# Kernel tuning notes

Hardware: AMD Instinct MI355X
Metric: run time of the kernel (lower is better)

## Reference

```python
import jax, jax.numpy as jnp
import numpy as np

EMBED = 1024
HEADS = 16
DK = EMBED // HEADS
DFF = 4 * EMBED
EPS = 1e-5


def layer_norm(x, g, b):
    mu = jnp.mean(x, axis=-1, keepdims=True)
    var = jnp.var(x, axis=-1, keepdims=True)
    return (x - mu) * jax.lax.rsqrt(var + EPS) * g + b


def setup_inputs() -> dict:
    key = jax.random.key(0)
    ks = jax.random.split(key, 12)
    s = lambda d: 1.0 / np.sqrt(d)
    return {
        "x": jax.random.normal(ks[0], (4, 1024, EMBED), dtype=jnp.float32),
        "norm_g": jnp.ones((EMBED,), jnp.float32),
        "norm_b": jnp.zeros((EMBED,), jnp.float32),
        "w_qkv": jax.random.normal(ks[1], (EMBED, 3 * EMBED), jnp.float32) * s(EMBED),
        "b_qkv": jnp.zeros((3 * EMBED,), jnp.float32),
        "w_proj": jax.random.normal(ks[2], (EMBED, EMBED), jnp.float32) * s(EMBED),
        "b_proj": jnp.zeros((EMBED,), jnp.float32),
        "w_fc1": jax.random.normal(ks[3], (EMBED, DFF), jnp.float32) * s(EMBED),
        "b_fc1": jnp.zeros((DFF,), jnp.float32),
        "w_fc2": jax.random.normal(ks[4], (DFF, EMBED), jnp.float32) * s(DFF),
        "b_fc2": jnp.zeros((EMBED,), jnp.float32),
    }


def reference(x, norm_g, norm_b, w_qkv, b_qkv, w_proj, b_proj, w_fc1, b_fc1, w_fc2, b_fc2):
    B, N, C = x.shape
    # --- attention branch (pre-norm, shared norm params) ---
    h = layer_norm(x, norm_g, norm_b)
    qkv = (h @ w_qkv + b_qkv).reshape(B, N, 3, HEADS, DK)
    q, k, v = jnp.moveaxis(qkv, 2, 0)  # each [B, N, H, dk]
    # NOTE: source divides by dk**(-0.5), i.e. multiplies scores by sqrt(dk)
    scores = jnp.einsum('bnhd,bmhd->bhnm', q, k) * (DK ** 0.5)
    attn = jax.nn.softmax(scores, axis=-1)
    ctx = jnp.einsum('bhnm,bmhd->bnhd', attn, v).reshape(B, N, C)
    x = x + (ctx @ w_proj + b_proj)
    # --- MLP branch ---
    h = layer_norm(x, norm_g, norm_b)
    h = jax.nn.gelu(h @ w_fc1 + b_fc1, approximate=False)
    x = x + (h @ w_fc2 + b_fc2)
    return x
```

## Files before the change

### kernel.cpp

```cpp
#include <hip/hip_runtime.h>
#include <hip/hip_bf16.h>

typedef __attribute__((ext_vector_type(8))) short short8;
typedef __attribute__((ext_vector_type(8))) _Float16 half8;
typedef __attribute__((ext_vector_type(4))) float f32x4;

__device__ __forceinline__ unsigned short f2h(float f) {
    _Float16 h = (_Float16)f;
    return *reinterpret_cast<unsigned short*>(&h);
}
__device__ __forceinline__ float h2f(unsigned short u) {
    _Float16 h = *reinterpret_cast<_Float16*>(&u);
    return (float)h;
}

__device__ __forceinline__ void gld_lds16(const unsigned short* g, unsigned short* l) {
    __builtin_amdgcn_global_load_lds(
        (const __attribute__((address_space(1))) unsigned int*)g,
        (__attribute__((address_space(3))) unsigned int*)l, 16, 0, 0);
}

__global__ __launch_bounds__(256)
void transpose_all(const float* __restrict__ W0, const float* __restrict__ W1,
                   const float* __restrict__ W2, const float* __restrict__ W3,
                   unsigned short* __restrict__ o0, unsigned short* __restrict__ o1,
                   unsigned short* __restrict__ o2, unsigned short* __restrict__ o3) {
    __shared__ float tile[32][33];
    const int bid = blockIdx.x;
    const float* W; unsigned short* out; int K, N, loc;
    if (bid < 3072)      { W = W0; out = o0; K = 1024; N = 3072; loc = bid; }
    else if (bid < 4096) { W = W1; out = o1; K = 1024; N = 1024; loc = bid - 3072; }
    else if (bid < 8192) { W = W2; out = o2; K = 1024; N = 4096; loc = bid - 4096; }
    else                 { W = W3; out = o3; K = 4096; N = 1024; loc = bid - 8192; }
    const int nx = N >> 5;
    const int n0 = (loc % nx) << 5, k0 = (loc / nx) << 5;
    const int tid = threadIdx.x;
    const int r = tid >> 3, c4 = (tid & 7) << 2;
    float4 v = *reinterpret_cast<const float4*>(W + (size_t)(k0 + r) * N + n0 + c4);
    tile[r][c4 + 0] = v.x; tile[r][c4 + 1] = v.y;
    tile[r][c4 + 2] = v.z; tile[r][c4 + 3] = v.w;
    __syncthreads();
    const int n = n0 + r;
    ushort4 o;
    o.x = f2h(tile[c4 + 0][r]); o.y = f2h(tile[c4 + 1][r]);
    o.z = f2h(tile[c4 + 2][r]); o.w = f2h(tile[c4 + 3][r]);
    *reinterpret_cast<ushort4*>(out + (size_t)n * K + k0 + c4) = o;
}

__global__ __launch_bounds__(256)
void ln_kernel(const float* __restrict__ x, const float* __restrict__ gw,
               const float* __restrict__ bw, unsigned short* __restrict__ out) {
    const int row = blockIdx.x, tid = threadIdx.x;
    const float* xr = x + (size_t)row * 1024;
    float4 v = *reinterpret_cast<const float4*>(xr + tid * 4);
    float s = v.x + v.y + v.z + v.w;
    float sq = v.x * v.x + v.y * v.y + v.z * v.z + v.w * v.w;
    #pragma unroll
    for (int off = 1; off < 64; off <<= 1) {
        s  += __shfl_xor(s, off);
        sq += __shfl_xor(sq, off);
    }
    __shared__ float ps[4], pq[4];
    const int wave = tid >> 6;
    if ((tid & 63) == 0) { ps[wave] = s; pq[wave] = sq; }
    __syncthreads();
    s  = ps[0] + ps[1] + ps[2] + ps[3];
    sq = pq[0] + pq[1] + pq[2] + pq[3];
    const float mu = s * (1.0f / 1024.0f);
    const float var = sq * (1.0f / 1024.0f) - mu * mu;
    const float rs = rsqrtf(var + 1e-5f);
    float4 gv = *reinterpret_cast<const float4*>(gw + tid * 4);
    float4 bv = *reinterpret_cast<const float4*>(bw + tid * 4);
    ushort4 o;
    o.x = f2h((v.x - mu) * rs * gv.x + bv.x);
    o.y = f2h((v.y - mu) * rs * gv.y + bv.y);
    o.z = f2h((v.z - mu) * rs * gv.z + bv.z);
    o.w = f2h((v.w - mu) * rs * gv.w + bv.w);
    *reinterpret_cast<ushort4*>(out + (size_t)row * 1024 + tid * 4) = o;
}

template<int EPI>
__global__ __launch_bounds__(512, 4)
void gemm_mid(const unsigned short* __restrict__ A, const unsigned short* __restrict__ Bt,
              const float* __restrict__ bias, void* Cout,
              int M, int N, int K, int lda, int ldb, int ldc) {
    __shared__ unsigned short As[2][128 * 32];
    __shared__ unsigned short Bs[2][256 * 32];
    const int tid = threadIdx.x;
    const int wave = tid >> 6, lane = tid & 63;
    const int nwg = gridDim.x;
    const int swz = (blockIdx.x & 7) * (nwg >> 3) + (blockIdx.x >> 3);
    const int nx = N >> 8;
    const int bm = (swz / nx) << 7, bn = (swz % nx) << 8;
    const int wm = wave >> 2, wn = wave & 3;
    const int fr = lane & 15, g8 = (lane >> 4) << 3, fq = (lane >> 4) << 2;
    const int jq = g8 >> 3;
    const int sx2 = (fr >> 1) & 3;

    const int srow = lane >> 2;
    const int scol = ((lane & 3) ^ ((lane >> 3) & 3)) << 3;
    const unsigned short* gA  = A + (size_t)(bm + wave * 16 + srow) * lda + scol;
    const unsigned short* gB0 = Bt + (size_t)(bn + wave * 32 + srow) * ldb + scol;
    const unsigned short* gB1 = gB0 + (size_t)16 * ldb;
    const int lbA = wave * 512;
    const int lbB = wave * 1024;

    f32x4 acc[4][4];
    #pragma unroll
    for (int m = 0; m < 4; ++m)
        #pragma unroll
        for (int n_ = 0; n_ < 4; ++n_)
            #pragma unroll
            for (int r_ = 0; r_ < 4; ++r_) acc[m][n_][r_] = 0.0f;

    auto stage = [&](int buf, int k0) {
        gld_lds16(gA + k0, &As[buf][lbA]);
        gld_lds16(gB0 + k0, &Bs[buf][lbB]);
        gld_lds16(gB1 + k0, &Bs[buf][lbB + 512]);
    };
    auto compute = [&](int buf) {
        half8 af[4], bfv[4];
        #pragma unroll
        for (int m = 0; m < 4; ++m)
            af[m] = *reinterpret_cast<const half8*>(
                &As[buf][(wm * 64 + m * 16 + fr) * 32 + ((jq ^ sx2) << 3)]);
        #pragma unroll
        for (int n_ = 0; n_ < 4; ++n_)
            bfv[n_] = *reinterpret_cast<const half8*>(
                &Bs[buf][(wn * 64 + n_ * 16 + fr) * 32 + ((jq ^ sx2) << 3)]);
        #pragma unroll
        for (int m = 0; m < 4; ++m)
            #pragma unroll
            for (int n_ = 0; n_ < 4; ++n_)
                acc[m][n_] = __builtin_amdgcn_mfma_f32_16x16x32_f16(af[m], bfv[n_], acc[m][n_], 0, 0, 0);
    };

    const int nt = K >> 5;
    stage(0, 0);
    __syncthreads();
    int k0 = 32;
    for (int t = 0; t < nt - 2; t += 2) {
        stage(1, k0);
        compute(0);
        __syncthreads();
        stage(0, k0 + 32);
        compute(1);
        __syncthreads();
        k0 += 64;
    }
    stage(1, k0);
    compute(0);
    __syncthreads();
    compute(1);

    unsigned short* o16 = reinterpret_cast<unsigned short*>(Cout);
    #pragma unroll
    for (int n_ = 0; n_ < 4; ++n_) {
        const int col = bn + wn * 64 + n_ * 16 + fr;
        const float bc = bias[col];
        #pragma unroll
        for (int m = 0; m < 4; ++m) {
            #pragma unroll
            for (int r_ = 0; r_ < 4; ++r_) {
                const int row = bm + wm * 64 + m * 16 + fq + r_;
                const size_t idx = (size_t)row * ldc + col;
                float v = acc[m][n_][r_] + bc;
                if (EPI == 0) {
                    o16[idx] = f2h(v);
                } else {
                    float ge = 0.5f * v * (1.0f + erff(v * 0.70710678118654752f));
                    o16[idx] = f2h(ge);
                }
            }
        }
    }
}

template<int EPI, int BM>
__global__ __launch_bounds__(256)
void gemm_bt(const unsigned short* __restrict__ A, const unsigned short* __restrict__ Bt,
             const float* __restrict__ bias, const float* resid,
             void* Cout, int M, int N, int K, int lda, int ldb, int ldc) {
    constexpr int MF = BM / 32;
    __shared__ unsigned short As[2][BM * 32];
    __shared__ unsigned short Bs[2][128 * 32];
    const int tid = threadIdx.x;
    const int wave = tid >> 6, lane = tid & 63;
    const int bm = blockIdx.y * BM, bn = blockIdx.x << 7;
    const int wr = (wave >> 1) * (BM / 2), wc = (wave & 1) << 6;
    const int fr = lane & 15, g8 = (lane >> 4) << 3, fq = (lane >> 4) << 2;
    const int jq = g8 >> 3, sx2 = (fr >> 1) & 3;
    const size_t koff = (EPI >= 3) ? (size_t)blockIdx.z * K : 0;

    const int srowA = (BM == 128) ? ((wave << 5) + (lane >> 2)) : ((wave << 4) + (lane >> 2));
    const int srowB = (wave << 5) + (lane >> 2);
    const int scol = (((lane & 3) ^ ((lane >> 3) & 3))) << 3;
    const unsigned short* gA0 = A + (size_t)(bm + srowA) * lda + scol + koff;
    const unsigned short* gA1 = gA0 + (size_t)16 * lda;
    const unsigned short* gB0 = Bt + (size_t)(bn + srowB) * ldb + scol + koff;
    const unsigned short* gB1 = gB0 + (size_t)16 * ldb;

    f32x4 acc[MF][4];
    #pragma unroll
    for (int m = 0; m < MF; ++m)
        #pragma unroll
        for (int n = 0; n < 4; ++n)
            #pragma unroll
            for (int r = 0; r < 4; ++r) acc[m][n][r] = 0.0f;

    auto stage = [&](int buf, int k0) {
        unsigned short* lA = &As[buf][(BM == 128) ? (wave << 10) : (wave << 9)];
        unsigned short* lB = &Bs[buf][wave << 10];
        gld_lds16(gA0 + k0, lA);
        if constexpr (BM == 128) gld_lds16(gA1 + k0, lA + 512);
        gld_lds16(gB0 + k0, lB);
        gld_lds16(gB1 + k0, lB + 512);
    };
    auto compute = [&](int buf) {
        half8 af[MF], bfv[4];
        #pragma unroll
        for (int m = 0; m < MF; ++m)
            af[m] = *reinterpret_cast<const half8*>(
                &As[buf][(wr + m * 16 + fr) * 32 + ((jq ^ sx2) << 3)]);
        #pragma unroll
        for (int n = 0; n < 4; ++n)
            bfv[n] = *reinterpret_cast<const half8*>(
                &Bs[buf][(wc + n * 16 + fr) * 32 + ((jq ^ sx2) << 3)]);
        #pragma unroll
        for (int m = 0; m < MF; ++m)
            #pragma unroll
            for (int n = 0; n < 4; ++n)
                acc[m][n] = __builtin_amdgcn_mfma_f32_16x16x32_f16(af[m], bfv[n], acc[m][n], 0, 0, 0);
    };

    const int nt = K >> 5;
    stage(0, 0);
    __syncthreads();
    int k0 = 32;
    for (int t = 0; t < nt - 2; t += 2) {
        stage(1, k0);
        compute(0);
        __syncthreads();
        stage(0, k0 + 32);
        compute(1);
        __syncthreads();
        k0 += 64;
    }
    stage(1, k0);
    compute(0);
    __syncthreads();
    compute(1);

    if (EPI == 4) {
        unsigned short* P = reinterpret_cast<unsigned short*>(Cout) +
                            (size_t)blockIdx.z * (size_t)M * ldc;
        #pragma unroll
        for (int n = 0; n < 4; ++n) {
            const int col = bn + wc + n * 16 + fr;
            #pragma unroll
            for (int m = 0; m < MF; ++m)
                #pragma unroll
                for (int r = 0; r < 4; ++r) {
                    const int row = bm + wr + m * 16 + fq + r;
                    P[(size_t)row * ldc + col] = f2h(acc[m][n][r]);
                }
        }
        return;
    }

    #pragma unroll
    for (int n = 0; n < 4; ++n) {
        const int col = bn + wc + n * 16 + fr;
        const float bc = bias[col];
        #pragma unroll
        for (int m = 0; m < MF; ++m) {
            #pragma unroll
            for (int r = 0; r < 4; ++r) {
                const int row = bm + wr + m * 16 + fq + r;
                const size_t idx = (size_t)row * ldc + col;
                float v = acc[m][n][r] + bc;
                reinterpret_cast<float*>(Cout)[idx] = v + resid[idx];
            }
        }
    }
}

template<int Z>
__global__ __launch_bounds__(256)
void red_h(const unsigned short* __restrict__ p, const float* __restrict__ bias,
           float* out) {
    const size_t MN = (size_t)4096 * 1024;
    const size_t i = ((size_t)blockIdx.x * 256 + threadIdx.x) * 4;
    float4 r  = *reinterpret_cast<const float4*>(out + i);
    float4 bb = *reinterpret_cast<const float4*>(bias + (i & 1023));
    float o0 = r.x + bb.x, o1 = r.y + bb.y, o2 = r.z + bb.z, o3 = r.w + bb.w;
    #pragma unroll
    for (int z = 0; z < Z; ++z) {
        ushort4 a = *reinterpret_cast<const ushort4*>(p + (size_t)z * MN + i);
        o0 += h2f(a.x); o1 += h2f(a.y); o2 += h2f(a.z); o3 += h2f(a.w);
    }
    float4 o; o.x = o0; o.y = o1; o.z = o2; o.w = o3;
    *reinterpret_cast<float4*>(out + i) = o;
}

__global__ __launch_bounds__(256)
void kv_conv(const unsigned short* __restrict__ qkv16, unsigned short* __restrict__ K_g,
             unsigned short* __restrict__ Vt_g) {
    __shared__ unsigned short VtT[64][72];
    const int kc = blockIdx.x;
    const int bh = blockIdx.y;
    const int b = bh >> 4, h = bh & 15;
    const int tid = threadIdx.x;
    const int key = tid >> 2, c16 = (tid & 3) << 4;
    const unsigned short* kp = qkv16 + ((size_t)(b * 1024 + kc * 64 + key)) * 3072 + 1024 + h * 64 + c16;
    alignas(16) unsigned short kbuf[16];
    #pragma unroll
    for (int j = 0; j < 16; j += 8) {
        short8 k8 = *reinterpret_cast<const short8*>(kp + j);
        short8 v8 = *reinterpret_cast<const short8*>(kp + 1024 + j);
        #pragma unroll
        for (int c = 0; c < 8; ++c) {
            kbuf[j + c] = f2h(8.0f * h2f((unsigned short)k8[c]));
            VtT[c16 + j + c][key] = (unsigned short)v8[c];
        }
    }
    const size_t kb = ((size_t)bh * 1024 + kc * 64 + key) * 64 + c16;
    *reinterpret_cast<short8*>(K_g + kb)     = *reinterpret_cast<short8*>(&kbuf[0]);
    *reinterpret_cast<short8*>(K_g + kb + 8) = *reinterpret_cast<short8*>(&kbuf[8]);
    __syncthreads();
    const int d = tid >> 2;
    const size_t vb = ((size_t)bh * 64 + d) * 1024 + (size_t)kc * 64 + c16;
    *reinterpret_cast<short8*>(Vt_g + vb)     = *reinterpret_cast<const short8*>(&VtT[d][c16]);
    *reinterpret_cast<short8*>(Vt_g + vb + 8) = *reinterpret_cast<const short8*>(&VtT[d][c16 + 8]);
}

__global__ __launch_bounds__(256)
void attn_kernel(const unsigned short* __restrict__ qkv16,
                 const unsigned short* __restrict__ K_g,
                 const unsigned short* __restrict__ Vt_g,
                 unsigned short* __restrict__ ctx) {
    __shared__ unsigned short Kh[64][72];
    __shared__ unsigned short Vt[64][72];
    __shared__ unsigned short Plds[4][16][72];
    const int qt = blockIdx.x;
    const int bh = blockIdx.y;
    const int b = bh >> 4, h = bh & 15;
    const int tid = threadIdx.x;
    const int wave = tid >> 6, lane = tid & 63;
    const int fr = lane & 15, g8 = (lane >> 4) << 3, fq = (lane >> 4) << 2;

    const int qrow = qt * 64 + wave * 16 + fr;
    const unsigned short* qp = qkv16 + ((size_t)(b * 1024 + qrow)) * 3072 + h * 64;
    half8 qf[2];
    qf[0] = *reinterpret_cast<const half8*>(qp + g8);
    qf[1] = *reinterpret_cast<const half8*>(qp + 32 + g8);

    float mrun[4], lrun[4];
    f32x4 cacc[4];
    #pragma unroll
    for (int r = 0; r < 4; ++r) { mrun[r] = -3.0e38f; lrun[r] = 0.0f; }
    #pragma unroll
    for (int nd = 0; nd < 4; ++nd)
        #pragma unroll
        for (int r = 0; r < 4; ++r) cacc[nd][r] = 0.0f;

    const int skey = tid >> 2, sc16 = (tid & 3) << 4;
    const unsigned short* kgp = K_g + ((size_t)bh * 1024 + skey) * 64 + sc16;
    const unsigned short* vgp = Vt_g + ((size_t)bh * 64 + skey) * 1024 + sc16;

    short8 ka = *reinterpret_cast<const short8*>(kgp);
    short8 kb = *reinterpret_cast<const short8*>(kgp + 8);
    short8 va = *reinterpret_cast<const short8*>(vgp);
    short8 vb = *reinterpret_cast<const short8*>(vgp + 8);

    for (int kt = 0; kt < 16; ++kt) {
        __syncthreads();
        *reinterpret_cast<short8*>(&Kh[skey][sc16])     = ka;
        *reinterpret_cast<short8*>(&Kh[skey][sc16 + 8]) = kb;
        *reinterpret_cast<short8*>(&Vt[skey][sc16])     = va;
        *reinterpret_cast<short8*>(&Vt[skey][sc16 + 8]) = vb;
        __syncthreads();
        const int ktn = (kt < 15) ? kt + 1 : 15;
        ka = *reinterpret_cast<const short8*>(kgp + (size_t)ktn * 4096);
        kb = *reinterpret_cast<const short8*>(kgp + (size_t)ktn * 4096 + 8);
        va = *reinterpret_cast<const short8*>(vgp + ktn * 64);
        vb = *reinterpret_cast<const short8*>(vgp + ktn * 64 + 8);

        f32x4 S[4];
        #pragma unroll
        for (int n = 0; n < 4; ++n)
            #pragma unroll
            for (int r = 0; r < 4; ++r) S[n][r] = 0.0f;
        #pragma unroll
        for (int s_ = 0; s_ < 2; ++s_)
            #pragma unroll
            for (int n = 0; n < 4; ++n) {
                half8 kh = *reinterpret_cast<const half8*>(&Kh[n * 16 + fr][s_ * 32 + g8]);
                S[n] = __builtin_amdgcn_mfma_f32_16x16x32_f16(qf[s_], kh, S[n], 0, 0, 0);
            }

        float mt[4];
        #pragma unroll
        for (int r = 0; r < 4; ++r)
            mt[r] = fmaxf(fmaxf(S[0][r], S[1][r]), fmaxf(S[2][r], S[3][r]));
        #pragma unroll
        for (int r = 0; r < 4; ++r) {
            mt[r] = fmaxf(mt[r], __shfl_xor(mt[r], 1));
            mt[r] = fmaxf(mt[r], __shfl_xor(mt[r], 2));
            mt[r] = fmaxf(mt[r], __shfl_xor(mt[r], 4));
            mt[r] = fmaxf(mt[r], __shfl_xor(mt[r], 8));
        }
        float P[4][4], rsum[4];
        #pragma unroll
        for (int r = 0; r < 4; ++r) {
            float mnew = fmaxf(mrun[r], mt[r]);
            float sf = __expf(mrun[r] - mnew);
            mrun[r] = mnew;
            rsum[r] = 0.0f;
            #pragma unroll
            for (int n = 0; n < 4; ++n) {
                float p = __expf(S[n][r] - mnew);
                P[n][r] = p;
                rsum[r] += p;
            }
            lrun[r] *= sf;
            #pragma unroll
            for (int nd = 0; nd < 4; ++nd) cacc[nd][r] *= sf;
        }
        #pragma unroll
        for (int r = 0; r < 4; ++r) {
            rsum[r] += __shfl_xor(rsum[r], 1);
            rsum[r] += __shfl_xor(rsum[r], 2);
            rsum[r] += __shfl_xor(rsum[r], 4);
            rsum[r] += __shfl_xor(rsum[r], 8);
            lrun[r] += rsum[r];
        }
        #pragma unroll
        for (int n = 0; n < 4; ++n)
            #pragma unroll
            for (int r = 0; r < 4; ++r)
                Plds[wave][fq + r][n * 16 + fr] = f2h(P[n][r]);
        #pragma unroll
        for (int s_ = 0; s_ < 2; ++s_) {
            half8 pa = *reinterpret_cast<const half8*>(&Plds[wave][fr][s_ * 32 + g8]);
            #pragma unroll
            for (int nd = 0; nd < 4; ++nd) {
                half8 vb8 = *reinterpret_cast<const half8*>(&Vt[nd * 16 + fr][s_ * 32 + g8]);
                cacc[nd] = __builtin_amdgcn_mfma_f32_16x16x32_f16(pa, vb8, cacc[nd], 0, 0, 0);
            }
        }
    }
    #pragma unroll
    for (int r = 0; r < 4; ++r) {
        const float inv = 1.0f / lrun[r];
        const int row = qt * 64 + wave * 16 + fq + r;
        unsigned short* cp = ctx + ((size_t)(b * 1024 + row)) * 1024 + h * 64;
        #pragma unroll
        for (int nd = 0; nd < 4; ++nd)
            cp[nd * 16 + fr] = f2h(cacc[nd][r] * inv);
    }
}

extern "C" void kernel_launch(void* const* d_in, const int* in_sizes, int n_in,
                              void* d_out, int out_size, void* d_ws, size_t ws_size,
                              hipStream_t stream) {
    const float* x      = (const float*)d_in[0];
    const float* norm_g = (const float*)d_in[1];
    const float* norm_b = (const float*)d_in[2];
    const float* w_qkv  = (const float*)d_in[3];
    const float* b_qkv  = (const float*)d_in[4];
    const float* w_proj = (const float*)d_in[5];
    const float* b_proj = (const float*)d_in[6];
    const float* w_fc1  = (const float*)d_in[7];
    const float* b_fc1  = (const float*)d_in[8];
    const float* w_fc2  = (const float*)d_in[9];
    const float* b_fc2  = (const float*)d_in[10];
    float* out = (float*)d_out;
    char* ws = (char*)d_ws;

    size_t off = 0;
    unsigned short* wqkvT  = (unsigned short*)(ws + off); off += (size_t)3072 * 1024 * 2;
    unsigned short* wprojT = (unsigned short*)(ws + off); off += (size_t)1024 * 1024 * 2;
    unsigned short* wfc1T  = (unsigned short*)(ws + off); off += (size_t)4096 * 1024 * 2;
    unsigned short* wfc2T  = (unsigned short*)(ws + off); off += (size_t)1024 * 4096 * 2;
    unsigned short* ctxb   = (unsigned short*)(ws + off); off += (size_t)4096 * 1024 * 2;
    char* G = ws + off;
    unsigned short* h1    = (unsigned short*)G;
    unsigned short* qkv16 = (unsigned short*)(G + (size_t)8388608);
    unsigned short* K_g   = (unsigned short*)G;
    unsigned short* Vt_g  = (unsigned short*)(G + (size_t)33554432);
    unsigned short* fc1o  = (unsigned short*)G;
    unsigned short* h2    = (unsigned short*)(G + (size_t)41943040);
    unsigned short* fc2ph = (unsigned short*)(G + (size_t)33554432);

    transpose_all<<<12288, 256, 0, stream>>>(w_qkv, w_proj, w_fc1, w_fc2,
                                             wqkvT, wprojT, wfc1T, wfc2T);

    ln_kernel<<<4096, 256, 0, stream>>>(x, norm_g, norm_b, h1);
    gemm_mid<0><<<384, 512, 0, stream>>>(h1, wqkvT, b_qkv, qkv16,
                                         4096, 3072, 1024, 1024, 1024, 3072);

    kv_conv<<<dim3(16, 64), 256, 0, stream>>>(qkv16, K_g, Vt_g);

    attn_kernel<<<dim3(16, 64), 256, 0, stream>>>(qkv16, K_g, Vt_g, ctxb);

    gemm_bt<1, 64><<<dim3(8, 64), 256, 0, stream>>>(ctxb, wprojT, b_proj, x, out,
                                                    4096, 1024, 1024, 1024, 1024, 1024);

    ln_kernel<<<4096, 256, 0, stream>>>(out, norm_g, norm_b, h2);
    gemm_mid<2><<<512, 512, 0, stream>>>(h2, wfc1T, b_fc1, fc1o,
                                         4096, 4096, 1024, 1024, 1024, 4096);

    gemm_bt<4, 64><<<dim3(8, 64, 4), 256, 0, stream>>>(fc1o, wfc2T, nullptr, nullptr, fc2ph,
                                                       4096, 1024, 1024, 4096, 4096, 1024);
    red_h<4><<<4096, 256, 0, stream>>>(fc2ph, b_fc2, out);
}
```

Baseline: 284.1 us.

## Run split-K FC2 on the larger 128x256 tile GEMM and remap blocks per XCD

The FC2 split-K GEMM moves from the 256-thread 64x128-tile kernel to the 512-thread 128x256-tile gemm_mid kernel, which gains a split-K z index and a partial-output epilogue. The larger tile gives more arithmetic per byte loaded. Block indices for FC2 and the projection GEMM are remapped so that each XCD gets consecutive M rows, which should improve L2 locality. The proj GEMM now launches on a 1D grid. Larger tiles give fewer blocks (512), which may reduce occupancy and load balance.

```diff
diff --git a/kernel.cpp b/kernel.cpp
--- a/kernel.cpp
+++ b/kernel.cpp
@@ -79,7 +79,7 @@
     *reinterpret_cast<ushort4*>(out + (size_t)row * 1024 + tid * 4) = o;
 }
 
-template<int EPI>
+template<int EPI, int NZ>
 __global__ __launch_bounds__(512, 4)
 void gemm_mid(const unsigned short* __restrict__ A, const unsigned short* __restrict__ Bt,
               const float* __restrict__ bias, void* Cout,
@@ -88,10 +88,20 @@
     __shared__ unsigned short Bs[2][256 * 32];
     const int tid = threadIdx.x;
     const int wave = tid >> 6, lane = tid & 63;
-    const int nwg = gridDim.x;
-    const int swz = (blockIdx.x & 7) * (nwg >> 3) + (blockIdx.x >> 3);
     const int nx = N >> 8;
-    const int bm = (swz / nx) << 7, bn = (swz % nx) << 8;
+    int bm, bn, z;
+    if (NZ == 1) {
+        const int nwg = gridDim.x;
+        const int swz = (blockIdx.x & 7) * (nwg >> 3) + (blockIdx.x >> 3);
+        bm = (swz / nx) << 7; bn = (swz % nx) << 8; z = 0;
+    } else {
+        int bid = blockIdx.x;
+        const int xcd = bid & 7; int rest = bid >> 3;
+        bn = (rest % nx) << 8; rest /= nx;
+        z = rest % NZ; rest /= NZ;
+        bm = (rest * 8 + xcd) << 7;
+    }
+    const size_t koff = (size_t)z * K;
     const int wm = wave >> 2, wn = wave & 3;
     const int fr = lane & 15, g8 = (lane >> 4) << 3, fq = (lane >> 4) << 2;
     const int jq = g8 >> 3;
@@ -99,8 +109,8 @@
 
     const int srow = lane >> 2;
     const int scol = ((lane & 3) ^ ((lane >> 3) & 3)) << 3;
-    const unsigned short* gA  = A + (size_t)(bm + wave * 16 + srow) * lda + scol;
-    const unsigned short* gB0 = Bt + (size_t)(bn + wave * 32 + srow) * ldb + scol;
+    const unsigned short* gA  = A + (size_t)(bm + wave * 16 + srow) * lda + scol + koff;
+    const unsigned short* gB0 = Bt + (size_t)(bn + wave * 32 + srow) * ldb + scol + koff;
     const unsigned short* gB1 = gB0 + (size_t)16 * ldb;
     const int lbA = wave * 512;
     const int lbB = wave * 1024;
@@ -152,6 +162,23 @@
     compute(0);
     __syncthreads();
     compute(1);
+
+    if (EPI == 4) {
+        unsigned short* P = reinterpret_cast<unsigned short*>(Cout) +
+                            (size_t)z * (size_t)M * ldc;
+        #pragma unroll
+        for (int n_ = 0; n_ < 4; ++n_) {
+            const int col = bn + wn * 64 + n_ * 16 + fr;
+            #pragma unroll
+            for (int m = 0; m < 4; ++m)
+                #pragma unroll
+                for (int r_ = 0; r_ < 4; ++r_) {
+                    const int row = bm + wm * 64 + m * 16 + fq + r_;
+                    P[(size_t)row * ldc + col] = f2h(acc[m][n_][r_]);
+                }
+        }
+        return;
+    }
 
     unsigned short* o16 = reinterpret_cast<unsigned short*>(Cout);
     #pragma unroll
@@ -176,7 +203,7 @@
     }
 }
 
-template<int EPI, int BM>
+template<int EPI, int BM, int REMAP>
 __global__ __launch_bounds__(256)
 void gemm_bt(const unsigned short* __restrict__ A, const unsigned short* __restrict__ Bt,
              const float* __restrict__ bias, const float* resid,
@@ -186,18 +213,26 @@
     __shared__ unsigned short Bs[2][128 * 32];
     const int tid = threadIdx.x;
     const int wave = tid >> 6, lane = tid & 63;
-    const int bm = blockIdx.y * BM, bn = blockIdx.x << 7;
+    int bm, bn;
+    if (REMAP) {
+        const int nxr = N >> 7;
+        int bid = blockIdx.x;
+        const int xcd = bid & 7; int rest = bid >> 3;
+        bn = (rest % nxr) << 7; rest /= nxr;
+        bm = (rest * 8 + xcd) * BM;
+    } else {
+        bm = blockIdx.y * BM; bn = blockIdx.x << 7;
+    }
     const int wr = (wave >> 1) * (BM / 2), wc = (wave & 1) << 6;
     const int fr = lane & 15, g8 = (lane >> 4) << 3, fq = (lane >> 4) << 2;
     const int jq = g8 >> 3, sx2 = (fr >> 1) & 3;
-    const size_t koff = (EPI >= 3) ? (size_t)blockIdx.z * K : 0;
 
     const int srowA = (BM == 128) ? ((wave << 5) + (lane >> 2)) : ((wave << 4) + (lane >> 2));
     const int srowB = (wave << 5) + (lane >> 2);
     const int scol = (((lane & 3) ^ ((lane >> 3) & 3))) << 3;
-    const unsigned short* gA0 = A + (size_t)(bm + srowA) * lda + scol + koff;
+    const unsigned short* gA0 = A + (size_t)(bm + srowA) * lda + scol;
     const unsigned short* gA1 = gA0 + (size_t)16 * lda;
-    const unsigned short* gB0 = Bt + (size_t)(bn + srowB) * ldb + scol + koff;
+    const unsigned short* gB0 = Bt + (size_t)(bn + srowB) * ldb + scol;
     const unsigned short* gB1 = gB0 + (size_t)16 * ldb;
 
     f32x4 acc[MF][4];
@@ -250,23 +285,6 @@
     compute(0);
     __syncthreads();
     compute(1);
-
-    if (EPI == 4) {
-        unsigned short* P = reinterpret_cast<unsigned short*>(Cout) +
-                            (size_t)blockIdx.z * (size_t)M * ldc;
-        #pragma unroll
-        for (int n = 0; n < 4; ++n) {
-            const int col = bn + wc + n * 16 + fr;
-            #pragma unroll
-            for (int m = 0; m < MF; ++m)
-                #pragma unroll
-                for (int r = 0; r < 4; ++r) {
-                    const int row = bm + wr + m * 16 + fq + r;
-                    P[(size_t)row * ldc + col] = f2h(acc[m][n][r]);
-                }
-        }
-        return;
-    }
 
     #pragma unroll
     for (int n = 0; n < 4; ++n) {
@@ -497,21 +515,21 @@
                                              wqkvT, wprojT, wfc1T, wfc2T);
 
     ln_kernel<<<4096, 256, 0, stream>>>(x, norm_g, norm_b, h1);
-    gemm_mid<0><<<384, 512, 0, stream>>>(h1, wqkvT, b_qkv, qkv16,
-                                         4096, 3072, 1024, 1024, 1024, 3072);
+    gemm_mid<0, 1><<<384, 512, 0, stream>>>(h1, wqkvT, b_qkv, qkv16,
+                                            4096, 3072, 1024, 1024, 1024, 3072);
 
     kv_conv<<<dim3(16, 64), 256, 0, stream>>>(qkv16, K_g, Vt_g);
 
     attn_kernel<<<dim3(16, 64), 256, 0, stream>>>(qkv16, K_g, Vt_g, ctxb);
 
-    gemm_bt<1, 64><<<dim3(8, 64), 256, 0, stream>>>(ctxb, wprojT, b_proj, x, out,
-                                                    4096, 1024, 1024, 1024, 1024, 1024);
+    gemm_bt<1, 64, 1><<<512, 256, 0, stream>>>(ctxb, wprojT, b_proj, x, out,
+                                               4096, 1024, 1024, 1024, 1024, 1024);
 
     ln_kernel<<<4096, 256, 0, stream>>>(out, norm_g, norm_b, h2);
-    gemm_mid<2><<<512, 512, 0, stream>>>(h2, wfc1T, b_fc1, fc1o,
-                                         4096, 4096, 1024, 1024, 1024, 4096);
-
-    gemm_bt<4, 64><<<dim3(8, 64, 4), 256, 0, stream>>>(fc1o, wfc2T, nullptr, nullptr, fc2ph,
-                                                       4096, 1024, 1024, 4096, 4096, 1024);
+    gemm_mid<2, 1><<<512, 512, 0, stream>>>(h2, wfc1T, b_fc1, fc1o,
+                                            4096, 4096, 1024, 1024, 1024, 4096);
+
+    gemm_mid<4, 4><<<512, 512, 0, stream>>>(fc1o, wfc2T, nullptr, fc2ph,
+                                            4096, 1024, 1024, 4096, 4096, 1024);
     red_h<4><<<4096, 256, 0, stream>>>(fc2ph, b_fc2, out);
 }
```

New measurement: 262.3 us. -7.7%, faster.
